# Optimization experiments

Hardware: AMD Instinct MI355X
Metric: run time of the kernel (lower is better)

## Reference

```python
import jax, jax.numpy as jnp
import numpy as np

P_DIM = 128
NV = 33000; NP_ = 33000; ND = 33000
N = NV + NP_ + ND            # 99000 nodes
E = 800000                    # edges
G = 64                        # graphs in batch
R = 4                         # message-passing iterations


def setup_inputs() -> dict:
    key = jax.random.key(0)
    ks = jax.random.split(key, 24)
    f = lambda k, s: jax.random.normal(k, s, dtype=jnp.float32)
    w = lambda k, s: 0.05 * jax.random.normal(k, s, dtype=jnp.float32)
    inp = {
        "edge_attr": f(ks[0], (E,)),
        "node_mu": f(ks[1], (N, P_DIM)),
        "x_vehicle": f(ks[2], (NV, 2)),
        "x_pickup": f(ks[3], (NP_, 3)),
        "x_dropoff": f(ks[4], (ND, 2)),
        # torch Linear weights stored as (in, out); y = x @ W + b
        "W1": w(ks[5], (P_DIM, P_DIM)), "b1": w(ks[6], (P_DIM,)),
        "W2": w(ks[7], (P_DIM, P_DIM)), "b2": w(ks[8], (P_DIM,)),
        "W3": w(ks[9], (1, P_DIM)),     "b3": w(ks[10], (P_DIM,)),
        "Wv": w(ks[11], (2, P_DIM)),    "bv": w(ks[12], (P_DIM,)),
        "Wp": w(ks[13], (3, P_DIM)),    "bp": w(ks[14], (P_DIM,)),
        "Wd": w(ks[15], (2, P_DIM)),    "bd": w(ks[16], (P_DIM,)),
        "Wc": w(ks[17], (P_DIM, 1)),    "bc": w(ks[18], (1,)),
        "edge_index": jax.random.randint(ks[19], (2, E), 0, N),
        # block layout: first NV vehicles (type 0), then pickups (1), dropoffs (2)
        "node_types": jnp.concatenate([
            jnp.zeros((NV,), jnp.int32),
            jnp.ones((NP_,), jnp.int32),
            jnp.full((ND,), 2, jnp.int32)]),
        "batch": jnp.sort(jax.random.randint(ks[20], (N,), 0, G)),
        "num_graphs": G,
    }
    return inp


def reference(edge_attr, node_mu, x_vehicle, x_pickup, x_dropoff,
              W1, b1, W2, b2, W3, b3, Wv, bv, Wp, bp, Wd, bd, Wc, bc,
              edge_index, node_types, batch, num_graphs):
    n_nodes = node_mu.shape[0]
    src, dst = edge_index[0], edge_index[1]

    # theta3 on edge attrs (constant across iterations -> hoisted, same math)
    t = jax.nn.leaky_relu(edge_attr[:, None] @ W3 + b3)          # (E, p)
    agg_t = jax.ops.segment_sum(t, dst, num_segments=n_nodes)    # (N, p)
    t_term = agg_t @ W2 + b2                                     # theta2 term

    # per-node-type additive transform; node types are laid out in blocks so
    # mu[mask] += Linear_t(x_t) is a block-ordered concat (constant per iter)
    type_add = jnp.concatenate([
        x_vehicle @ Wv + bv,
        x_pickup @ Wp + bp,
        x_dropoff @ Wd + bd], axis=0)                            # (N, p)

    mu = node_mu
    for _ in range(R):
        agg_mu = jax.ops.segment_sum(mu[src], dst, num_segments=n_nodes)
        mu = jax.nn.leaky_relu(agg_mu @ W1 + b1 + t_term + type_add)

    # scatter_mean over graph ids
    g_sum = jax.ops.segment_sum(mu, batch, num_segments=num_graphs)
    counts = jax.ops.segment_sum(jnp.ones((n_nodes,), mu.dtype), batch,
                                 num_segments=num_graphs)
    g = g_sum / jnp.maximum(counts, 1.0)[:, None]                # (G, p)
    proba = jax.nn.sigmoid(g @ Wc + bc)                          # (G, 1)
    return proba
```

## Files before the change

### kernel.cpp

```cpp
#include <hip/hip_runtime.h>
#include <math.h>

#define P 128

typedef __attribute__((ext_vector_type(8))) short short8;
typedef __attribute__((ext_vector_type(4))) float f32x4;

static __device__ __forceinline__ float lrelu(float x){ return x > 0.f ? x : 0.01f*x; }
static __device__ __forceinline__ float bflo(unsigned u){ union{unsigned u; float f;} c; c.u = u << 16; return c.f; }
static __device__ __forceinline__ float bfhi(unsigned u){ union{unsigned u; float f;} c; c.u = u & 0xffff0000u; return c.f; }
static __device__ __forceinline__ unsigned fbits(float f){ union{float f; unsigned u;} c; c.f = f; return c.u; }
static __device__ __forceinline__ unsigned packbf(float x, float y){
  unsigned ux = fbits(x); ux += 0x7fffu + ((ux >> 16) & 1u);
  unsigned uy = fbits(y); uy += 0x7fffu + ((uy >> 16) & 1u);
  return (ux >> 16) | (uy & 0xffff0000u);
}

__global__ void k_hist(const int* __restrict__ dst, int E, int* __restrict__ cnt){
  for(int i = blockIdx.x*blockDim.x + threadIdx.x; i < E; i += gridDim.x*blockDim.x)
    atomicAdd(&cnt[dst[i]], 1);
}

__global__ void k_scan1(const int* __restrict__ cnt, int N, int* __restrict__ off, int* __restrict__ partial){
  __shared__ int s[256];
  int t = threadIdx.x, i = blockIdx.x*256 + t;
  int v = (i < N) ? cnt[i] : 0;
  s[t] = v; __syncthreads();
  for(int o = 1; o < 256; o <<= 1){
    int x = (t >= o) ? s[t-o] : 0; __syncthreads();
    s[t] += x; __syncthreads();
  }
  if(i < N) off[i] = s[t];
  if(t == 255) partial[blockIdx.x] = s[255];
}

__global__ void k_scan2(int* __restrict__ partial, int nb){
  __shared__ int s[512];
  int t = threadIdx.x;
  int v = (t < nb) ? partial[t] : 0;
  s[t] = v; __syncthreads();
  for(int o = 1; o < 512; o <<= 1){
    int x = (t >= o) ? s[t-o] : 0; __syncthreads();
    s[t] += x; __syncthreads();
  }
  if(t < nb) partial[t] = s[t] - v;
}

__global__ void k_scan3(const int* __restrict__ cnt, int N, int E, int* __restrict__ off, const int* __restrict__ partial){
  int i = blockIdx.x*256 + threadIdx.x;
  if(i < N) off[i] = off[i] - cnt[i] + partial[blockIdx.x];
  if(i == 0) off[N] = E;
}

__global__ void k_scatter(const int* __restrict__ ei, const float* __restrict__ ea, int E,
                          const int* __restrict__ off, int* __restrict__ cur,
                          int* __restrict__ csr_src, float* __restrict__ csr_attr){
  const int* src = ei; const int* dst = ei + E;
  for(int i = blockIdx.x*blockDim.x + threadIdx.x; i < E; i += gridDim.x*blockDim.x){
    int d = dst[i];
    int p = off[d] + atomicAdd(&cur[d], 1);
    csr_src[p]  = src[i];
    csr_attr[p] = ea[i];
  }
}

__global__ void k_cvt(const float2* __restrict__ in, unsigned* __restrict__ out, int n){
  int i = blockIdx.x*256 + threadIdx.x;
  if(i < n){ float2 v = in[i]; out[i] = packbf(v.x, v.y); }
}

__global__ void k_transW(const float* __restrict__ W1, const float* __restrict__ W2,
                         unsigned* __restrict__ W1T, unsigned* __restrict__ W2T){
  int b = blockIdx.x;
  const float* W = (b < 128) ? W1 : W2;
  unsigned* WT   = (b < 128) ? W1T : W2T;
  int j = b & 127, k2 = threadIdx.x;
  float a = W[(size_t)(2*k2)*P + j], c = W[(size_t)(2*k2+1)*P + j];
  WT[(size_t)j*64 + k2] = packbf(a, c);
}

__global__ __launch_bounds__(512) void k_gemmB(
    const int* __restrict__ off, const float* __restrict__ csr_attr,
    const float* __restrict__ W3, const float* __restrict__ b3,
    const short8* __restrict__ WT,
    const float* __restrict__ b1, const float* __restrict__ b2,
    const float* __restrict__ xv, const float* __restrict__ Wv, const float* __restrict__ bv,
    const float* __restrict__ xp, const float* __restrict__ Wp, const float* __restrict__ bp,
    const float* __restrict__ xd, const float* __restrict__ Wd, const float* __restrict__ bd,
    int NV, int NP_, int N, unsigned* __restrict__ Out){
  __shared__ __align__(16) float shf[64*132];
  __shared__ float spar[1408];
  int t = threadIdx.x, w = t >> 6, l = t & 63;
  int bm = blockIdx.x * 64;
  unsigned* Albs = (unsigned*)shf;

  for(int i = t; i < 1408; i += 512){
    float v;
    if(i < 128)       v = b1[i] + b2[i];
    else if(i < 384)  v = Wv[i-128];
    else if(i < 512)  v = bv[i-384];
    else if(i < 896)  v = Wp[i-512];
    else if(i < 1024) v = bp[i-896];
    else if(i < 1280) v = Wd[i-1024];
    else              v = bd[i-1280];
    spar[i] = v;
  }

  float w0 = W3[2*l], w1 = W3[2*l+1];
  float c0 = b3[2*l], c1 = b3[2*l+1];
  for(int i = 0; i < 8; ++i){
    int node = bm + w*8 + i;
    float a0 = 0.f, a1 = 0.f;
    if(node < N){
      int s0 = off[node], s1 = off[node+1];
      for(int p = s0; p < s1; ++p){
        float a = csr_attr[p];
        a0 += lrelu(fmaf(a, w0, c0));
        a1 += lrelu(fmaf(a, w1, c1));
      }
    }
    int row = w*8 + i;
    Albs[(row*256 + ((l*4) ^ ((row&7)<<4))) >> 2] = packbf(a0, a1);
  }
  __syncthreads();

  int lr = l & 15, lg = l >> 4;
  int wm = w & 3, wn = w >> 2;
  f32x4 acc[4];
  #pragma unroll
  for(int i = 0; i < 4; ++i) acc[i] = (f32x4)0.f;
  int arow = wm*16 + lr;
  #pragma unroll
  for(int ks = 0; ks < 4; ++ks){
    short8 a = *(const short8*)((const char*)shf + arow*256 + ((((ks*4+lg)*16) ^ ((arow&7)<<4))));
    #pragma unroll
    for(int ct = 0; ct < 4; ++ct){
      short8 b = WT[(size_t)(wn*64 + ct*16 + lr)*16 + ks*4 + lg];
      acc[ct] = __builtin_amdgcn_mfma_f32_16x16x32_bf16(a, b, acc[ct], 0, 0, 0);
    }
  }
  __syncthreads();
  #pragma unroll
  for(int ct = 0; ct < 4; ++ct)
    #pragma unroll
    for(int r = 0; r < 4; ++r)
      shf[(wm*16 + lg*4 + r)*132 + wn*64 + ct*16 + lr] = acc[ct][r];
  __syncthreads();

  int r = t >> 3, seg8 = t & 7;
  int row = bm + r;
  if(row >= N) return;
  float x0, x1, x2; int ty;
  if(row < NV){ ty = 0; x0 = xv[2*row]; x1 = xv[2*row+1]; x2 = 0.f; }
  else if(row < NV + NP_){ int i2 = row - NV; ty = 1; x0 = xp[3*i2]; x1 = xp[3*i2+1]; x2 = xp[3*i2+2]; }
  else { int i2 = row - NV - NP_; ty = 2; x0 = xd[2*i2]; x1 = xd[2*i2+1]; x2 = 0.f; }
  const float4* s4 = (const float4*)&shf[r*132 + seg8*16];
  float sv[16];
  #pragma unroll
  for(int q = 0; q < 4; ++q){ float4 v = s4[q]; sv[4*q]=v.x; sv[4*q+1]=v.y; sv[4*q+2]=v.z; sv[4*q+3]=v.w; }
  unsigned o[8];
  #pragma unroll
  for(int i = 0; i < 8; ++i){
    int c = seg8*16 + 2*i;
    float f0 = sv[2*i]   + spar[c];
    float f1 = sv[2*i+1] + spar[c+1];
    if(ty == 0){
      f0 += spar[384+c]   + x0*spar[128+c]   + x1*spar[256+c];
      f1 += spar[384+c+1] + x0*spar[128+c+1] + x1*spar[256+c+1];
    } else if(ty == 1){
      f0 += spar[896+c]   + x0*spar[512+c]   + x1*spar[640+c]   + x2*spar[768+c];
      f1 += spar[896+c+1] + x0*spar[512+c+1] + x1*spar[640+c+1] + x2*spar[768+c+1];
    } else {
      f0 += spar[1280+c]   + x0*spar[1024+c]   + x1*spar[1152+c];
      f1 += spar[1280+c+1] + x0*spar[1024+c+1] + x1*spar[1152+c+1];
    }
    o[i] = packbf(f0, f1);
  }
  uint4* dst = (uint4*)(Out + (size_t)row*64 + seg8*8);
  dst[0] = make_uint4(o[0], o[1], o[2], o[3]);
  dst[1] = make_uint4(o[4], o[5], o[6], o[7]);
}

__global__ __launch_bounds__(512) void k_fused(
    const int* __restrict__ off, const int* __restrict__ csr_src,
    const unsigned* __restrict__ mu, const short8* __restrict__ WT,
    const unsigned* __restrict__ baseB, unsigned* __restrict__ Out, int N){
  __shared__ __align__(16) float shf[64*132];
  int t = threadIdx.x, w = t >> 6, l = t & 63;
  int bm = blockIdx.x * 64;
  unsigned* Albs = (unsigned*)shf;

  for(int i = 0; i < 8; ++i){
    int node = bm + w*8 + i;
    float x0=0.f,y0=0.f,x1=0.f,y1=0.f,x2=0.f,y2=0.f,x3=0.f,y3=0.f;
    if(node < N){
      int s0 = off[node], s1 = off[node+1];
      int p = s0;
      for(; p+3 < s1; p += 4){
        unsigned v0 = mu[(size_t)csr_src[p]*64 + l];
        unsigned v1 = mu[(size_t)csr_src[p+1]*64 + l];
        unsigned v2 = mu[(size_t)csr_src[p+2]*64 + l];
        unsigned v3 = mu[(size_t)csr_src[p+3]*64 + l];
        x0 += bflo(v0); y0 += bfhi(v0);
        x1 += bflo(v1); y1 += bfhi(v1);
        x2 += bflo(v2); y2 += bfhi(v2);
        x3 += bflo(v3); y3 += bfhi(v3);
      }
      for(; p < s1; ++p){
        unsigned v = mu[(size_t)csr_src[p]*64 + l];
        x0 += bflo(v); y0 += bfhi(v);
      }
    }
    int row = w*8 + i;
    Albs[(row*256 + ((l*4) ^ ((row&7)<<4))) >> 2] = packbf(x0+x1+x2+x3, y0+y1+y2+y3);
  }
  __syncthreads();

  int lr = l & 15, lg = l >> 4;
  int wm = w & 3, wn = w >> 2;
  f32x4 acc[4];
  #pragma unroll
  for(int i = 0; i < 4; ++i) acc[i] = (f32x4)0.f;
  int arow = wm*16 + lr;
  #pragma unroll
  for(int ks = 0; ks < 4; ++ks){
    short8 a = *(const short8*)((const char*)shf + arow*256 + ((((ks*4+lg)*16) ^ ((arow&7)<<4))));
    #pragma unroll
    for(int ct = 0; ct < 4; ++ct){
      short8 b = WT[(size_t)(wn*64 + ct*16 + lr)*16 + ks*4 + lg];
      acc[ct] = __builtin_amdgcn_mfma_f32_16x16x32_bf16(a, b, acc[ct], 0, 0, 0);
    }
  }
  __syncthreads();
  #pragma unroll
  for(int ct = 0; ct < 4; ++ct)
    #pragma unroll
    for(int r = 0; r < 4; ++r)
      shf[(wm*16 + lg*4 + r)*132 + wn*64 + ct*16 + lr] = acc[ct][r];
  __syncthreads();

  int r = t >> 3, seg8 = t & 7;
  int row = bm + r;
  if(row >= N) return;
  const float4* s4 = (const float4*)&shf[r*132 + seg8*16];
  float sv[16];
  #pragma unroll
  for(int q = 0; q < 4; ++q){ float4 v = s4[q]; sv[4*q]=v.x; sv[4*q+1]=v.y; sv[4*q+2]=v.z; sv[4*q+3]=v.w; }
  const unsigned* ad = baseB + (size_t)row*64 + seg8*8;
  unsigned o[8];
  #pragma unroll
  for(int i = 0; i < 8; ++i){
    unsigned b = ad[i];
    float f0 = lrelu(sv[2*i]   + bflo(b));
    float f1 = lrelu(sv[2*i+1] + bfhi(b));
    o[i] = packbf(f0, f1);
  }
  uint4* dst = (uint4*)(Out + (size_t)row*64 + seg8*8);
  dst[0] = make_uint4(o[0], o[1], o[2], o[3]);
  dst[1] = make_uint4(o[4], o[5], o[6], o[7]);
}

#define GSB 256
__global__ void k_gsum(const unsigned* __restrict__ mu, const int* __restrict__ batch, int N,
                       float* __restrict__ gsum){
  int c = threadIdx.x & 63, sub = threadIdx.x >> 6;
  int n0 = blockIdx.x * GSB;
  int n1 = min(n0 + GSB, N);
  float ax = 0.f, ay = 0.f; int curg = -1;
  for(int n = n0 + sub; n < n1; n += 4){
    int g = batch[n];
    if(g != curg){
      if(curg >= 0){ atomicAdd(&gsum[curg*P + 2*c], ax); atomicAdd(&gsum[curg*P + 2*c + 1], ay); }
      curg = g; ax = 0.f; ay = 0.f;
    }
    unsigned v = mu[(size_t)n*64 + c];
    ax += bflo(v); ay += bfhi(v);
  }
  if(curg >= 0){ atomicAdd(&gsum[curg*P + 2*c], ax); atomicAdd(&gsum[curg*P + 2*c + 1], ay); }
}

__global__ void k_out(const float* __restrict__ gsum, const int* __restrict__ batch, int N,
                      const float* __restrict__ Wc, const float* __restrict__ bc,
                      float* __restrict__ out){
  int g = blockIdx.x, t = threadIdx.x;
  int lo = 0, hi = N;
  while(lo < hi){ int m=(lo+hi)>>1; if(batch[m] < g) lo = m+1; else hi = m; }
  int start = lo; lo = start; hi = N;
  while(lo < hi){ int m=(lo+hi)>>1; if(batch[m] <= g) lo = m+1; else hi = m; }
  int cnt = lo - start;
  float cf = cnt < 1 ? 1.f : (float)cnt;
  __shared__ float red[128];
  red[t] = (gsum[g*P + t] / cf) * Wc[t];
  __syncthreads();
  for(int o = 64; o > 0; o >>= 1){ if(t < o) red[t] += red[t+o]; __syncthreads(); }
  if(t == 0) out[g] = 1.f/(1.f + expf(-(red[0] + bc[0])));
}

extern "C" void kernel_launch(void* const* d_in, const int* in_sizes, int n_in,
                              void* d_out, int out_size, void* d_ws, size_t ws_size,
                              hipStream_t stream){
  const float* edge_attr = (const float*)d_in[0];
  const float* node_mu   = (const float*)d_in[1];
  const float* xv = (const float*)d_in[2];
  const float* xp = (const float*)d_in[3];
  const float* xd = (const float*)d_in[4];
  const float* W1 = (const float*)d_in[5];  const float* b1 = (const float*)d_in[6];
  const float* W2 = (const float*)d_in[7];  const float* b2 = (const float*)d_in[8];
  const float* W3 = (const float*)d_in[9];  const float* b3 = (const float*)d_in[10];
  const float* Wv = (const float*)d_in[11]; const float* bv = (const float*)d_in[12];
  const float* Wp = (const float*)d_in[13]; const float* bp = (const float*)d_in[14];
  const float* Wd = (const float*)d_in[15]; const float* bd = (const float*)d_in[16];
  const float* Wc = (const float*)d_in[17]; const float* bc = (const float*)d_in[18];
  const int*   ei    = (const int*)d_in[19];
  const int*   batch = (const int*)d_in[21];
  const int E   = in_sizes[0];
  const int N   = in_sizes[1] / P;
  const int NV  = in_sizes[2] / 2;
  const int NP_ = in_sizes[3] / 3;
  const int G   = 64;
  float* out = (float*)d_out;

  char* w = (char*)d_ws; size_t o = 0;
  auto alloc = [&](size_t bytes)->void*{ size_t a = (o + 255) & ~(size_t)255; o = a + bytes; return (void*)(w + a); };
  int*      cnt      = (int*)     alloc((size_t)N*4);
  int*      cur      = (int*)     alloc((size_t)N*4);
  int*      off      = (int*)     alloc((size_t)(N+1)*4);
  int*      partial  = (int*)     alloc(512*4);
  int*      csr_src  = (int*)     alloc((size_t)E*4);
  float*    csr_attr = (float*)   alloc((size_t)E*4);
  unsigned* mu0      = (unsigned*)alloc((size_t)N*64*4);
  unsigned* YA       = (unsigned*)alloc((size_t)N*64*4);
  unsigned* YB       = (unsigned*)alloc((size_t)N*64*4);
  unsigned* baseB    = (unsigned*)alloc((size_t)N*64*4);
  unsigned* W1T      = (unsigned*)alloc((size_t)P*64*4);
  unsigned* W2T      = (unsigned*)alloc((size_t)P*64*4);
  float*    gsum     = (float*)   alloc((size_t)G*P*4);

  hipMemsetAsync(cnt,  0, (size_t)N*4, stream);
  hipMemsetAsync(cur,  0, (size_t)N*4, stream);
  hipMemsetAsync(gsum, 0, (size_t)G*P*4, stream);

  int nb = (N + 255) / 256;
  k_hist   <<<2048, 256, 0, stream>>>(ei + E, E, cnt);
  k_scan1  <<<nb,   256, 0, stream>>>(cnt, N, off, partial);
  k_scan2  <<<1,    512, 0, stream>>>(partial, nb);
  k_scan3  <<<nb,   256, 0, stream>>>(cnt, N, E, off, partial);
  k_scatter<<<2048, 256, 0, stream>>>(ei, edge_attr, E, off, cur, csr_src, csr_attr);

  int nhalf = N*64;
  k_cvt   <<<(nhalf + 255)/256, 256, 0, stream>>>((const float2*)node_mu, mu0, nhalf);
  k_transW<<<256, 64, 0, stream>>>(W1, W2, W1T, W2T);

  int ggemm = (N + 63) / 64;
  k_gemmB<<<ggemm, 512, 0, stream>>>(off, csr_attr, W3, b3, (const short8*)W2T,
                                     b1, b2, xv, Wv, bv, xp, Wp, bp, xd, Wd, bd,
                                     NV, NP_, N, baseB);

  k_fused<<<ggemm, 512, 0, stream>>>(off, csr_src, mu0, (const short8*)W1T, baseB, YA, N);
  k_fused<<<ggemm, 512, 0, stream>>>(off, csr_src, YA,  (const short8*)W1T, baseB, YB, N);
  k_fused<<<ggemm, 512, 0, stream>>>(off, csr_src, YB,  (const short8*)W1T, baseB, YA, N);
  k_fused<<<ggemm, 512, 0, stream>>>(off, csr_src, YA,  (const short8*)W1T, baseB, YB, N);

  k_gsum<<<(N + GSB - 1)/GSB, 256, 0, stream>>>(YB, batch, N, gsum);
  k_out <<<G, P, 0, stream>>>(gsum, batch, N, Wc, bc, out);
}
```

Before: 652.6 us.

## Fold type-linear terms into MFMA and halve epilogue LDS in gemm kernels

Folds the per-node-type linear transforms and biases into an extra bf16 MFMA k-step in k_gemmB, using a prepacked augmented weight block (W2Tx) and a per-row feature/one-hot vector in LDS. Both k_gemmB and k_fused now stage the accumulator epilogue through LDS in two column halves, shrinking shared memory from 64x132 to 64x68 floats to raise occupancy. Also unrolls the edge-attr accumulation and merges two memsets into one. Rounding the type weights and biases to bf16 adds precision loss, and the split epilogue needs extra barriers.

```diff
diff --git a/kernel.cpp b/kernel.cpp
--- a/kernel.cpp
+++ b/kernel.cpp
@@ -69,58 +69,94 @@
   if(i < n){ float2 v = in[i]; out[i] = packbf(v.x, v.y); }
 }
 
-__global__ void k_transW(const float* __restrict__ W1, const float* __restrict__ W2,
-                         unsigned* __restrict__ W1T, unsigned* __restrict__ W2T){
-  int b = blockIdx.x;
-  const float* W = (b < 128) ? W1 : W2;
-  unsigned* WT   = (b < 128) ? W1T : W2T;
-  int j = b & 127, k2 = threadIdx.x;
-  float a = W[(size_t)(2*k2)*P + j], c = W[(size_t)(2*k2+1)*P + j];
-  WT[(size_t)j*64 + k2] = packbf(a, c);
+__global__ void k_wprep(const float* __restrict__ W1, const float* __restrict__ W2,
+                        unsigned* __restrict__ W1T, unsigned* __restrict__ W2T,
+                        const float* __restrict__ Wv, const float* __restrict__ bv,
+                        const float* __restrict__ Wp, const float* __restrict__ bp,
+                        const float* __restrict__ Wd, const float* __restrict__ bd,
+                        const float* __restrict__ b1, const float* __restrict__ b2,
+                        unsigned* __restrict__ W2Tx){
+  int b = blockIdx.x, t = threadIdx.x;
+  if(b < 256){
+    if(t < 64){
+      const float* W = (b < 128) ? W1 : W2;
+      unsigned* WT   = (b < 128) ? W1T : W2T;
+      int j = b & 127, k2 = t;
+      float a = W[(size_t)(2*k2)*P + j], c = W[(size_t)(2*k2+1)*P + j];
+      WT[(size_t)j*64 + k2] = packbf(a, c);
+    }
+  } else {
+    int j = t;
+    unsigned q[16];
+    #pragma unroll
+    for(int i = 0; i < 16; ++i) q[i] = 0;
+    q[0] = packbf(Wv[j],     Wv[128+j]);
+    q[1] = packbf(Wp[j],     Wp[128+j]);
+    q[2] = packbf(Wp[256+j], Wd[j]);
+    q[3] = packbf(Wd[128+j], b1[j] + b2[j]);
+    q[4] = packbf(bv[j],     bp[j]);
+    q[5] = packbf(bd[j],     0.f);
+    uint4* dst = (uint4*)(W2Tx + (size_t)j*16);
+    #pragma unroll
+    for(int i = 0; i < 4; ++i) dst[i] = make_uint4(q[4*i], q[4*i+1], q[4*i+2], q[4*i+3]);
+  }
 }
 
 __global__ __launch_bounds__(512) void k_gemmB(
     const int* __restrict__ off, const float* __restrict__ csr_attr,
     const float* __restrict__ W3, const float* __restrict__ b3,
-    const short8* __restrict__ WT,
-    const float* __restrict__ b1, const float* __restrict__ b2,
-    const float* __restrict__ xv, const float* __restrict__ Wv, const float* __restrict__ bv,
-    const float* __restrict__ xp, const float* __restrict__ Wp, const float* __restrict__ bp,
-    const float* __restrict__ xd, const float* __restrict__ Wd, const float* __restrict__ bd,
+    const short8* __restrict__ WT, const short8* __restrict__ WTx,
+    const float* __restrict__ xv, const float* __restrict__ xp, const float* __restrict__ xd,
     int NV, int NP_, int N, unsigned* __restrict__ Out){
-  __shared__ __align__(16) float shf[64*132];
-  __shared__ float spar[1408];
+  __shared__ __align__(16) unsigned shu[5376];
   int t = threadIdx.x, w = t >> 6, l = t & 63;
   int bm = blockIdx.x * 64;
-  unsigned* Albs = (unsigned*)shf;
-
-  for(int i = t; i < 1408; i += 512){
-    float v;
-    if(i < 128)       v = b1[i] + b2[i];
-    else if(i < 384)  v = Wv[i-128];
-    else if(i < 512)  v = bv[i-384];
-    else if(i < 896)  v = Wp[i-512];
-    else if(i < 1024) v = bp[i-896];
-    else if(i < 1280) v = Wd[i-1024];
-    else              v = bd[i-1280];
-    spar[i] = v;
-  }
-
-  float w0 = W3[2*l], w1 = W3[2*l+1];
-  float c0 = b3[2*l], c1 = b3[2*l+1];
-  for(int i = 0; i < 8; ++i){
-    int node = bm + w*8 + i;
-    float a0 = 0.f, a1 = 0.f;
+
+  {
+    float w0 = W3[2*l], w1 = W3[2*l+1];
+    float c0 = b3[2*l], c1 = b3[2*l+1];
+    for(int i = 0; i < 8; ++i){
+      int row = w*8 + i, node = bm + row;
+      float a0=0.f, a1=0.f, g0=0.f, g1=0.f;
+      if(node < N){
+        int s0 = off[node], s1 = off[node+1];
+        int p = s0;
+        for(; p+3 < s1; p += 4){
+          float e0 = csr_attr[p], e1 = csr_attr[p+1], e2 = csr_attr[p+2], e3 = csr_attr[p+3];
+          a0 += lrelu(fmaf(e0, w0, c0)); a1 += lrelu(fmaf(e0, w1, c1));
+          g0 += lrelu(fmaf(e1, w0, c0)); g1 += lrelu(fmaf(e1, w1, c1));
+          a0 += lrelu(fmaf(e2, w0, c0)); a1 += lrelu(fmaf(e2, w1, c1));
+          g0 += lrelu(fmaf(e3, w0, c0)); g1 += lrelu(fmaf(e3, w1, c1));
+        }
+        for(; p < s1; ++p){
+          float e = csr_attr[p];
+          a0 += lrelu(fmaf(e, w0, c0)); a1 += lrelu(fmaf(e, w1, c1));
+        }
+      }
+      shu[(row*256 + ((l*4) ^ ((row&7)<<4))) >> 2] = packbf(a0+g0, a1+g1);
+    }
+  }
+  {
+    int r = t >> 3, q = t & 7;
+    int node = bm + r;
+    float x0=0.f, x1=0.f, x2=0.f; int ty = 3;
     if(node < N){
-      int s0 = off[node], s1 = off[node+1];
-      for(int p = s0; p < s1; ++p){
-        float a = csr_attr[p];
-        a0 += lrelu(fmaf(a, w0, c0));
-        a1 += lrelu(fmaf(a, w1, c1));
-      }
-    }
-    int row = w*8 + i;
-    Albs[(row*256 + ((l*4) ^ ((row&7)<<4))) >> 2] = packbf(a0, a1);
+      if(node < NV){ ty = 0; x0 = xv[2*node]; x1 = xv[2*node+1]; }
+      else if(node < NV + NP_){ int i2 = node - NV; ty = 1; x0 = xp[3*i2]; x1 = xp[3*i2+1]; x2 = xp[3*i2+2]; }
+      else { int i2 = node - NV - NP_; ty = 2; x0 = xd[2*i2]; x1 = xd[2*i2+1]; }
+    }
+    float s0v, s1v;
+    switch(q){
+      case 0: s0v = (ty==0)?x0:0.f; s1v = (ty==0)?x1:0.f; break;
+      case 1: s0v = (ty==1)?x0:0.f; s1v = (ty==1)?x1:0.f; break;
+      case 2: s0v = (ty==1)?x2:0.f; s1v = (ty==2)?x0:0.f; break;
+      case 3: s0v = (ty==2)?x1:0.f; s1v = (node<N)?1.f:0.f; break;
+      case 4: s0v = (ty==0)?1.f:0.f; s1v = (ty==1)?1.f:0.f; break;
+      case 5: s0v = (ty==2)?1.f:0.f; s1v = 0.f; break;
+      default: s0v = 0.f; s1v = 0.f; break;
+    }
+    shu[4096 + r*20 + q]     = packbf(s0v, s1v);
+    shu[4096 + r*20 + 8 + q] = 0u;
   }
   __syncthreads();
 
@@ -132,66 +168,57 @@
   int arow = wm*16 + lr;
   #pragma unroll
   for(int ks = 0; ks < 4; ++ks){
-    short8 a = *(const short8*)((const char*)shf + arow*256 + ((((ks*4+lg)*16) ^ ((arow&7)<<4))));
+    short8 a = *(const short8*)((const char*)shu + arow*256 + ((((ks*4+lg)*16) ^ ((arow&7)<<4))));
     #pragma unroll
     for(int ct = 0; ct < 4; ++ct){
       short8 b = WT[(size_t)(wn*64 + ct*16 + lr)*16 + ks*4 + lg];
       acc[ct] = __builtin_amdgcn_mfma_f32_16x16x32_bf16(a, b, acc[ct], 0, 0, 0);
     }
   }
-  __syncthreads();
-  #pragma unroll
-  for(int ct = 0; ct < 4; ++ct)
-    #pragma unroll
-    for(int r = 0; r < 4; ++r)
-      shf[(wm*16 + lg*4 + r)*132 + wn*64 + ct*16 + lr] = acc[ct][r];
-  __syncthreads();
-
-  int r = t >> 3, seg8 = t & 7;
+  {
+    short8 a = *(const short8*)&shu[4096 + arow*20 + lg*4];
+    #pragma unroll
+    for(int ct = 0; ct < 4; ++ct){
+      short8 b = WTx[(size_t)(wn*64 + ct*16 + lr)*4 + lg];
+      acc[ct] = __builtin_amdgcn_mfma_f32_16x16x32_bf16(a, b, acc[ct], 0, 0, 0);
+    }
+  }
+  __syncthreads();
+
+  float* shf = (float*)shu;
+  int r = t >> 3, seg = t & 7;
   int row = bm + r;
-  if(row >= N) return;
-  float x0, x1, x2; int ty;
-  if(row < NV){ ty = 0; x0 = xv[2*row]; x1 = xv[2*row+1]; x2 = 0.f; }
-  else if(row < NV + NP_){ int i2 = row - NV; ty = 1; x0 = xp[3*i2]; x1 = xp[3*i2+1]; x2 = xp[3*i2+2]; }
-  else { int i2 = row - NV - NP_; ty = 2; x0 = xd[2*i2]; x1 = xd[2*i2+1]; x2 = 0.f; }
-  const float4* s4 = (const float4*)&shf[r*132 + seg8*16];
-  float sv[16];
-  #pragma unroll
-  for(int q = 0; q < 4; ++q){ float4 v = s4[q]; sv[4*q]=v.x; sv[4*q+1]=v.y; sv[4*q+2]=v.z; sv[4*q+3]=v.w; }
-  unsigned o[8];
-  #pragma unroll
-  for(int i = 0; i < 8; ++i){
-    int c = seg8*16 + 2*i;
-    float f0 = sv[2*i]   + spar[c];
-    float f1 = sv[2*i+1] + spar[c+1];
-    if(ty == 0){
-      f0 += spar[384+c]   + x0*spar[128+c]   + x1*spar[256+c];
-      f1 += spar[384+c+1] + x0*spar[128+c+1] + x1*spar[256+c+1];
-    } else if(ty == 1){
-      f0 += spar[896+c]   + x0*spar[512+c]   + x1*spar[640+c]   + x2*spar[768+c];
-      f1 += spar[896+c+1] + x0*spar[512+c+1] + x1*spar[640+c+1] + x2*spar[768+c+1];
-    } else {
-      f0 += spar[1280+c]   + x0*spar[1024+c]   + x1*spar[1152+c];
-      f1 += spar[1280+c+1] + x0*spar[1024+c+1] + x1*spar[1152+c+1];
-    }
-    o[i] = packbf(f0, f1);
-  }
-  uint4* dst = (uint4*)(Out + (size_t)row*64 + seg8*8);
-  dst[0] = make_uint4(o[0], o[1], o[2], o[3]);
-  dst[1] = make_uint4(o[4], o[5], o[6], o[7]);
+  #pragma unroll
+  for(int h = 0; h < 2; ++h){
+    if(wn == h){
+      #pragma unroll
+      for(int ct = 0; ct < 4; ++ct)
+        #pragma unroll
+        for(int rr = 0; rr < 4; ++rr)
+          shf[(wm*16 + lg*4 + rr)*68 + ct*16 + lr] = acc[ct][rr];
+    }
+    __syncthreads();
+    if(row < N){
+      float4 v0 = *(const float4*)&shf[r*68 + seg*8];
+      float4 v1 = *(const float4*)&shf[r*68 + seg*8 + 4];
+      *(uint4*)&Out[(size_t)row*64 + h*32 + seg*4] =
+        make_uint4(packbf(v0.x,v0.y), packbf(v0.z,v0.w), packbf(v1.x,v1.y), packbf(v1.z,v1.w));
+    }
+    __syncthreads();
+  }
 }
 
 __global__ __launch_bounds__(512) void k_fused(
     const int* __restrict__ off, const int* __restrict__ csr_src,
     const unsigned* __restrict__ mu, const short8* __restrict__ WT,
     const unsigned* __restrict__ baseB, unsigned* __restrict__ Out, int N){
-  __shared__ __align__(16) float shf[64*132];
+  __shared__ __align__(16) float shf[64*68];
   int t = threadIdx.x, w = t >> 6, l = t & 63;
   int bm = blockIdx.x * 64;
   unsigned* Albs = (unsigned*)shf;
 
   for(int i = 0; i < 8; ++i){
-    int node = bm + w*8 + i;
+    int row = w*8 + i, node = bm + row;
     float x0=0.f,y0=0.f,x1=0.f,y1=0.f,x2=0.f,y2=0.f,x3=0.f,y3=0.f;
     if(node < N){
       int s0 = off[node], s1 = off[node+1];
@@ -211,7 +238,6 @@
         x0 += bflo(v); y0 += bfhi(v);
       }
     }
-    int row = w*8 + i;
     Albs[(row*256 + ((l*4) ^ ((row&7)<<4))) >> 2] = packbf(x0+x1+x2+x3, y0+y1+y2+y3);
   }
   __syncthreads();
@@ -232,32 +258,32 @@
     }
   }
   __syncthreads();
-  #pragma unroll
-  for(int ct = 0; ct < 4; ++ct)
-    #pragma unroll
-    for(int r = 0; r < 4; ++r)
-      shf[(wm*16 + lg*4 + r)*132 + wn*64 + ct*16 + lr] = acc[ct][r];
-  __syncthreads();
-
-  int r = t >> 3, seg8 = t & 7;
+
+  int r = t >> 3, seg = t & 7;
   int row = bm + r;
-  if(row >= N) return;
-  const float4* s4 = (const float4*)&shf[r*132 + seg8*16];
-  float sv[16];
-  #pragma unroll
-  for(int q = 0; q < 4; ++q){ float4 v = s4[q]; sv[4*q]=v.x; sv[4*q+1]=v.y; sv[4*q+2]=v.z; sv[4*q+3]=v.w; }
-  const unsigned* ad = baseB + (size_t)row*64 + seg8*8;
-  unsigned o[8];
-  #pragma unroll
-  for(int i = 0; i < 8; ++i){
-    unsigned b = ad[i];
-    float f0 = lrelu(sv[2*i]   + bflo(b));
-    float f1 = lrelu(sv[2*i+1] + bfhi(b));
-    o[i] = packbf(f0, f1);
-  }
-  uint4* dst = (uint4*)(Out + (size_t)row*64 + seg8*8);
-  dst[0] = make_uint4(o[0], o[1], o[2], o[3]);
-  dst[1] = make_uint4(o[4], o[5], o[6], o[7]);
+  #pragma unroll
+  for(int h = 0; h < 2; ++h){
+    if(wn == h){
+      #pragma unroll
+      for(int ct = 0; ct < 4; ++ct)
+        #pragma unroll
+        for(int rr = 0; rr < 4; ++rr)
+          shf[(wm*16 + lg*4 + rr)*68 + ct*16 + lr] = acc[ct][rr];
+    }
+    __syncthreads();
+    if(row < N){
+      float4 v0 = *(const float4*)&shf[r*68 + seg*8];
+      float4 v1 = *(const float4*)&shf[r*68 + seg*8 + 4];
+      const unsigned* ad = baseB + (size_t)row*64 + h*32 + seg*4;
+      unsigned b0 = ad[0], b1u = ad[1], b2u = ad[2], b3u = ad[3];
+      *(uint4*)&Out[(size_t)row*64 + h*32 + seg*4] = make_uint4(
+        packbf(lrelu(v0.x + bflo(b0)),  lrelu(v0.y + bfhi(b0))),
+        packbf(lrelu(v0.z + bflo(b1u)), lrelu(v0.w + bfhi(b1u))),
+        packbf(lrelu(v1.x + bflo(b2u)), lrelu(v1.y + bfhi(b2u))),
+        packbf(lrelu(v1.z + bflo(b3u)), lrelu(v1.w + bfhi(b3u))));
+    }
+    __syncthreads();
+  }
 }
 
 #define GSB 256
@@ -322,8 +348,7 @@
 
   char* w = (char*)d_ws; size_t o = 0;
   auto alloc = [&](size_t bytes)->void*{ size_t a = (o + 255) & ~(size_t)255; o = a + bytes; return (void*)(w + a); };
-  int*      cnt      = (int*)     alloc((size_t)N*4);
-  int*      cur      = (int*)     alloc((size_t)N*4);
+  int*      cntcur   = (int*)     alloc((size_t)2*N*4);
   int*      off      = (int*)     alloc((size_t)(N+1)*4);
   int*      partial  = (int*)     alloc(512*4);
   int*      csr_src  = (int*)     alloc((size_t)E*4);
@@ -334,11 +359,12 @@
   unsigned* baseB    = (unsigned*)alloc((size_t)N*64*4);
   unsigned* W1T      = (unsigned*)alloc((size_t)P*64*4);
   unsigned* W2T      = (unsigned*)alloc((size_t)P*64*4);
+  unsigned* W2Tx     = (unsigned*)alloc((size_t)P*16*4);
   float*    gsum     = (float*)   alloc((size_t)G*P*4);
-
-  hipMemsetAsync(cnt,  0, (size_t)N*4, stream);
-  hipMemsetAsync(cur,  0, (size_t)N*4, stream);
-  hipMemsetAsync(gsum, 0, (size_t)G*P*4, stream);
+  int* cnt = cntcur; int* cur = cntcur + N;
+
+  hipMemsetAsync(cntcur, 0, (size_t)2*N*4, stream);
+  hipMemsetAsync(gsum,   0, (size_t)G*P*4, stream);
 
   int nb = (N + 255) / 256;
   k_hist   <<<2048, 256, 0, stream>>>(ei + E, E, cnt);
@@ -348,13 +374,13 @@
   k_scatter<<<2048, 256, 0, stream>>>(ei, edge_attr, E, off, cur, csr_src, csr_attr);
 
   int nhalf = N*64;
-  k_cvt   <<<(nhalf + 255)/256, 256, 0, stream>>>((const float2*)node_mu, mu0, nhalf);
-  k_transW<<<256, 64, 0, stream>>>(W1, W2, W1T, W2T);
+  k_cvt  <<<(nhalf + 255)/256, 256, 0, stream>>>((const float2*)node_mu, mu0, nhalf);
+  k_wprep<<<257, 128, 0, stream>>>(W1, W2, W1T, W2T, Wv, bv, Wp, bp, Wd, bd, b1, b2, W2Tx);
 
   int ggemm = (N + 63) / 64;
-  k_gemmB<<<ggemm, 512, 0, stream>>>(off, csr_attr, W3, b3, (const short8*)W2T,
-                                     b1, b2, xv, Wv, bv, xp, Wp, bp, xd, Wd, bd,
-                                     NV, NP_, N, baseB);
+  k_gemmB<<<ggemm, 512, 0, stream>>>(off, csr_attr, W3, b3,
+                                     (const short8*)W2T, (const short8*)W2Tx,
+                                     xv, xp, xd, NV, NP_, N, baseB);
 
   k_fused<<<ggemm, 512, 0, stream>>>(off, csr_src, mu0, (const short8*)W1T, baseB, YA, N);
   k_fused<<<ggemm, 512, 0, stream>>>(off, csr_src, YA,  (const short8*)W1T, baseB, YB, N);
```

New measurement: 630.9 us. -3.3%, faster.
